# Optimization experiments

Hardware: AMD Instinct MI355X
Metric: run time of the kernel (lower is better)

The kernel has to match this reference:

```python
import jax, jax.numpy as jnp
import numpy as np

N = 100000      # nodes
E = 800000      # edges
IN1 = 128       # gcn input feature dim
IN2 = 64        # lstm input feature dim
H = 128         # hidden_channels
B = 32          # lstm batch
T = 200         # lstm seq len
OUT = 1         # out_channels
TARGET = jnp.array([0, 1000, 2000, 3000, 4000, 5000, 6000, 7000])  # numgcnE=8


def setup_inputs() -> dict:
    key = jax.random.key(0)
    ks = jax.random.split(key, 20)
    s = 0.05
    inp = {
        "data0": jax.random.normal(ks[0], (B, T, IN2), jnp.float32),
        "data1": jax.random.normal(ks[1], (N, IN1), jnp.float32),
        "edge_index": jax.random.randint(ks[2], (2, E), 0, N, dtype=jnp.int64),
        # GCNConv layers (weight stored [in, out])
        "W1": jax.random.normal(ks[3], (IN1, H), jnp.float32) * s,
        "b1": jnp.zeros((H,), jnp.float32),
        "W2": jax.random.normal(ks[4], (H, H), jnp.float32) * s,
        "b2": jnp.zeros((H,), jnp.float32),
        # LSTM1 (gate order i,f,g,o as in torch)
        "Wih1": jax.random.normal(ks[5], (4 * H, IN2), jnp.float32) * s,
        "Whh1": jax.random.normal(ks[6], (4 * H, H), jnp.float32) * s,
        "bih1": jnp.zeros((4 * H,), jnp.float32),
        "bhh1": jnp.zeros((4 * H,), jnp.float32),
        # LSTM2
        "Wih2": jax.random.normal(ks[7], (4 * H, H), jnp.float32) * s,
        "Whh2": jax.random.normal(ks[8], (4 * H, H), jnp.float32) * s,
        "bih2": jnp.zeros((4 * H,), jnp.float32),
        "bhh2": jnp.zeros((4 * H,), jnp.float32),
        # MLP head: (numgcnE+1)*H -> (numgcnE+1)*H/2 -> OUT
        "m1_w": jax.random.normal(ks[9], (9 * H, 9 * H // 2), jnp.float32) * s,
        "m1_b": jnp.zeros((9 * H // 2,), jnp.float32),
        "m2_w": jax.random.normal(ks[10], (9 * H // 2, OUT), jnp.float32) * s,
        "m2_b": jnp.zeros((OUT,), jnp.float32),
    }
    return inp


def gcn_conv(x, W, b, src, dst, n):
    # PyG GCNConv: self-loops + symmetric normalization, then scatter-add.
    xw = x @ W                                                     # [N, H]
    ones = jnp.ones(src.shape[0], xw.dtype)
    deg = jax.ops.segment_sum(ones, dst, num_segments=n) + 1.0     # +1 self-loop
    dinv = jax.lax.rsqrt(deg)                                      # [N]
    norm = dinv[src] * dinv[dst]                                   # [E]
    agg = jax.ops.segment_sum(xw[src] * norm[:, None], dst, num_segments=n)
    agg = agg + xw * (dinv * dinv)[:, None]                        # self-loop msgs
    return agg + b


def lstm_final(x_tbi, Wih, Whh, bih, bhh):
    # x_tbi: [T, Bsz, in]; returns final hidden state h_T [Bsz, H]
    Bsz = x_tbi.shape[1]
    Hh = Whh.shape[1]
    bias = bih + bhh

    def step(carry, xt):
        h, c = carry
        g = xt @ Wih.T + h @ Whh.T + bias                          # [Bsz, 4H]
        i, f, gg, o = jnp.split(g, 4, axis=-1)
        c = jax.nn.sigmoid(f) * c + jax.nn.sigmoid(i) * jnp.tanh(gg)
        h = jax.nn.sigmoid(o) * jnp.tanh(c)
        return (h, c), None

    init = (jnp.zeros((Bsz, Hh), x_tbi.dtype), jnp.zeros((Bsz, Hh), x_tbi.dtype))
    (h, c), _ = jax.lax.scan(step, init, x_tbi)
    return h


def reference(data0, data1, edge_index, W1, b1, W2, b2,
              Wih1, Whh1, bih1, bhh1, Wih2, Whh2, bih2, bhh2,
              m1_w, m1_b, m2_w, m2_b):
    src, dst = edge_index[0], edge_index[1]
    n = data1.shape[0]
    # two GCN layers with ReLU
    h = jax.nn.relu(gcn_conv(data1, W1, b1, src, dst, n))
    h = jax.nn.relu(gcn_conv(h, W2, b2, src, dst, n))
    g = h[TARGET].reshape(-1)                                      # [numgcnE*H]
    # lstm1 over [B, T, IN2] (batch_first) -> final h_n [B, H]
    h1 = lstm_final(jnp.swapaxes(data0, 0, 1), Wih1, Whh1, bih1, bhh1)
    # lstm2 consumes h_n[None] as [batch=1, seq=B, H] -> final h [1, H]
    h2 = lstm_final(h1[:, None, :], Wih2, Whh2, bih2, bhh2)[0]     # [H]
    d = jnp.concatenate([g, h2])                                   # [(numgcnE+1)*H]
    return (d @ m1_w + m1_b) @ m2_w + m2_b                         # [OUT]
```

## Files before the change

kernel.cpp:

```cpp
#include <hip/hip_runtime.h>
#include <hip/hip_bf16.h>
#include <cstring>

using bf16 = __hip_bfloat16;
typedef _Float16 h2v __attribute__((ext_vector_type(2)));
typedef _Float16 h8v __attribute__((ext_vector_type(8)));

#if __has_builtin(__builtin_amdgcn_fdot2)
__device__ __forceinline__ float FDOT2(h2v a, h2v b, float c) {
    return __builtin_amdgcn_fdot2(a, b, c, false);
}
#else
__device__ __forceinline__ float FDOT2(h2v a, h2v b, float c) {
    return c + (float)a.x * (float)b.x + (float)a.y * (float)b.y;
}
#endif

__device__ __forceinline__ float sigm_f(float x) {
    return __builtin_amdgcn_rcpf(1.f + __expf(-x));
}
__device__ __forceinline__ float tanh_f(float x) {
    return 1.f - 2.f * __builtin_amdgcn_rcpf(1.f + __expf(2.f * x));
}

constexpr int NH    = 128;
constexpr int G4    = 512;
constexpr int TSEQ  = 200;
constexpr int BBATCH= 32;
constexpr int NTGT  = 8;

constexpr int LCAP1 = 1024;
constexpr int S1CAP = LCAP1 + NTGT;
constexpr int LCAP2 = 8192;
constexpr int S2CAP = LCAP2 + S1CAP;

constexpr size_t algn(size_t x) { return (x + 255) & ~size_t(255); }
constexpr size_t OFF_GX1  = 0;
constexpr size_t OFF_GX2  = algn(OFF_GX1  + 6400ull * G4 * 4);
constexpr size_t OFF_DEG  = algn(OFF_GX2  + 32ull * G4 * 4);
constexpr size_t OFF_DINV = algn(OFF_DEG  + 100000ull * 4);
constexpr size_t OFF_SL1  = algn(OFF_DINV + 100000ull * 4);
constexpr size_t OFF_SL2  = algn(OFF_SL1  + 100000ull * 4);
constexpr size_t OFF_CNT  = algn(OFF_SL2  + 100000ull * 4);
constexpr size_t OFF_L1   = algn(OFF_CNT  + 64);
constexpr size_t OFF_S1   = algn(OFF_L1   + (size_t)LCAP1 * 8);
constexpr size_t OFF_L2   = algn(OFF_S1   + (size_t)S1CAP * 4);
constexpr size_t OFF_S2   = algn(OFF_L2   + (size_t)LCAP2 * 8);
constexpr size_t OFF_XW1  = algn(OFF_S2   + (size_t)S2CAP * 4);
constexpr size_t OFF_H1   = algn(OFF_XW1  + (size_t)S2CAP * NH * 4);
constexpr size_t OFF_XW2  = algn(OFF_H1   + (size_t)S1CAP * NH * 4);
constexpr size_t OFF_DVEC = algn(OFF_XW2  + (size_t)S1CAP * NH * 4);
constexpr size_t OFF_H1F  = algn(OFF_DVEC + 1152ull * 4);
constexpr size_t OFF_CACC = algn(OFF_H1F  + 32ull * NH * 4);
constexpr size_t WS_NEEDED = OFF_CACC + 576ull * 4;

__device__ __forceinline__ int edge_at(const int* ei, int E, int is64, int row, int e) {
    return is64 ? ei[(((size_t)row * E) + e) * 2] : ei[((size_t)row * E) + e];
}

__global__ void k_canary(unsigned int* out, unsigned int bits) {
    if (threadIdx.x == 0) out[0] = bits;
}


__global__ void k_init(const int* ei, int* deg, int* slot1, int* slot2, int* cnt,
                       float* colacc, int n) {
    int i = blockIdx.x * 256 + threadIdx.x;
    if (i < 14) cnt[i] = 0;
    if (i == 15) cnt[15] = (ei[1] == 0 && ei[3] == 0 && ei[5] == 0 && ei[7] == 0) ? 1 : 0;
    if (i < 576) colacc[i] = 0.f;
    for (; i < n; i += gridDim.x * 256) { deg[i] = 0; slot1[i] = -1; slot2[i] = -1; }
}

__global__ void k_deg_l1(const int* ei, int E, int* deg, int2* l1, int* cnt) {
    int is64 = cnt[15];
    for (int e = blockIdx.x * 256 + threadIdx.x; e < E; e += gridDim.x * 256) {
        int d = edge_at(ei, E, is64, 1, e);
        if ((unsigned)d < 100000u) atomicAdd(&deg[d], 1);
        if (d <= 7000 && d >= 0 && d % 1000 == 0) {
            int s = edge_at(ei, E, is64, 0, e);
            int idx = atomicAdd(&cnt[0], 1);
            if (idx < LCAP1) l1[idx] = make_int2(s, d);
        }
    }
}

__global__ void k_dinv(const int* deg, float* dinv, int n) {
    for (int i = blockIdx.x * 256 + threadIdx.x; i < n; i += gridDim.x * 256)
        dinv[i] = rsqrtf((float)deg[i] + 1.0f);
}

__global__ void k_s1(const int2* l1, int* cnt, int* slot1, int* s1list) {
    int m = min(cnt[0], LCAP1);
    for (int i = threadIdx.x; i < NTGT + m; i += blockDim.x) {
        int v = (i < NTGT) ? i * 1000 : l1[i - NTGT].x;
        if ((unsigned)v >= 100000u) continue;
        int old = atomicCAS(&slot1[v], -1, -2);
        if (old == -1) {
            int idx = atomicAdd(&cnt[1], 1);
            if (idx < S1CAP) { s1list[idx] = v; atomicExch(&slot1[v], idx); }
        }
    }
}

__global__ void k_s2self(const int* s1list, int* cnt, int* slot2, int* s2list) {
    int nS1 = min(cnt[1], S1CAP);
    for (int i = blockIdx.x * 256 + threadIdx.x; i < nS1; i += gridDim.x * 256) {
        int v = s1list[i];
        int old = atomicCAS(&slot2[v], -1, -2);
        if (old == -1) {
            int idx = atomicAdd(&cnt[2], 1);
            if (idx < S2CAP) { s2list[idx] = v; atomicExch(&slot2[v], idx); }
        }
    }
}

__global__ void k_l2(const int* ei, int E, const int* slot1,
                     int2* l2, int* cnt, int* slot2, int* s2list) {
    int is64 = cnt[15];
    for (int e = blockIdx.x * 256 + threadIdx.x; e < E; e += gridDim.x * 256) {
        int d = edge_at(ei, E, is64, 1, e);
        if ((unsigned)d >= 100000u) continue;
        if (slot1[d] >= 0) {
            int s = edge_at(ei, E, is64, 0, e);
            if ((unsigned)s >= 100000u) continue;
            int idx = atomicAdd(&cnt[3], 1);
            if (idx < LCAP2) l2[idx] = make_int2(s, d);
            int old = atomicCAS(&slot2[s], -1, -2);
            if (old == -1) {
                int j = atomicAdd(&cnt[2], 1);
                if (j < S2CAP) { s2list[j] = s; atomicExch(&slot2[s], j); }
            }
        }
    }
}


__global__ void k_xw1(const float* x, const float* W, const int* s2list, const int* cnt, float* xw1) {
    int i = blockIdx.x;
    if (i >= min(cnt[2], S2CAP)) return;
    int node = s2list[i];
    __shared__ float xs[NH];
    int c = threadIdx.x;
    xs[c] = x[(size_t)node * NH + c];
    __syncthreads();
    float acc = 0.f;
    #pragma unroll 8
    for (int k = 0; k < NH; k++) acc += xs[k] * W[(size_t)k * NH + c];
    xw1[(size_t)i * NH + c] = acc;
}

__global__ void k_h1init(const float* xw1, const int* s1list, const int* cnt,
                         const int* slot2, const float* dinv, float* h1) {
    int i = blockIdx.x;
    if (i >= min(cnt[1], S1CAP)) return;
    int node = s1list[i];
    int s2 = slot2[node];
    if (s2 < 0 || s2 >= S2CAP) s2 = 0;
    float v = dinv[node];
    h1[i * NH + threadIdx.x] = xw1[(size_t)s2 * NH + threadIdx.x] * v * v;
}

__global__ void k_h1scat(const float* xw1, const int2* l2, const int* cnt,
                         const int* slot1, const int* slot2, const float* dinv, float* h1) {
    int e = blockIdx.x;
    if (e >= min(cnt[3], LCAP2)) return;
    int2 sd = l2[e];
    int t1 = slot1[sd.y], s2 = slot2[sd.x];
    if (t1 < 0 || t1 >= S1CAP || s2 < 0 || s2 >= S2CAP) return;
    float w = dinv[sd.x] * dinv[sd.y];
    atomicAdd(&h1[t1 * NH + threadIdx.x],
              xw1[(size_t)s2 * NH + threadIdx.x] * w);
}

__global__ void k_xw2(const float* h1, const float* W, const float* b1, const int* cnt, float* xw2) {
    int i = blockIdx.x;
    if (i >= min(cnt[1], S1CAP)) return;
    __shared__ float xs[NH];
    int c = threadIdx.x;
    xs[c] = fmaxf(h1[i * NH + c] + b1[c], 0.f);
    __syncthreads();
    float acc = 0.f;
    #pragma unroll 8
    for (int k = 0; k < NH; k++) acc += xs[k] * W[(size_t)k * NH + c];
    xw2[(size_t)i * NH + c] = acc;
}

__global__ void k_gout(const float* xw2, const int2* l1, const int* cnt,
                       const int* slot1, const float* dinv, const float* b2, float* dvec) {
    int t = blockIdx.x;
    int tgt = t * 1000;
    int c = threadIdx.x;
    float vt = dinv[tgt];
    int st = slot1[tgt]; if (st < 0 || st >= S1CAP) st = 0;
    float acc = xw2[(size_t)st * NH + c] * vt * vt;
    int m = min(cnt[0], LCAP1);
    for (int e = 0; e < m; e++) {
        int2 sd = l1[e];
        if (sd.y == tgt) {
            int ss = slot1[sd.x];
            if (ss >= 0 && ss < S1CAP)
                acc += xw2[(size_t)ss * NH + c] * dinv[sd.x] * vt;
        }
    }
    acc += b2[c];
    dvec[t * NH + c] = fmaxf(acc, 0.f);
}


__global__ __launch_bounds__(256) void k_gx1(const float* data0, const float* Wih,
                                             const float* bih, const float* bhh, float* gx) {
    constexpr int LDP = 68;
    __shared__ float As[64 * LDP];
    __shared__ float Bs[64 * LDP];
    int tid = threadIdx.x;
    int rb = blockIdx.x >> 3;
    int gb = blockIdx.x & 7;
    int r0 = rb * 64, g0 = gb * 64;
    for (int i = tid; i < 64 * 64; i += 256) {
        int rr = i >> 6, k = i & 63;
        int r = r0 + rr, b = r & 31, t = r >> 5;
        As[rr * LDP + k] = data0[((size_t)b * TSEQ + t) * 64 + k];
        Bs[rr * LDP + k] = Wih[(size_t)(g0 + rr) * 64 + k];
    }
    __syncthreads();
    int tr = (tid & 15) * 4;
    int tg = (tid >> 4) * 4;
    float acc[4][4] = {};
    #pragma unroll
    for (int k4 = 0; k4 < 16; k4++) {
        float4 a0 = *(const float4*)&As[(tr + 0) * LDP + k4 * 4];
        float4 a1 = *(const float4*)&As[(tr + 1) * LDP + k4 * 4];
        float4 a2 = *(const float4*)&As[(tr + 2) * LDP + k4 * 4];
        float4 a3 = *(const float4*)&As[(tr + 3) * LDP + k4 * 4];
        float4 b0 = *(const float4*)&Bs[(tg + 0) * LDP + k4 * 4];
        float4 b1 = *(const float4*)&Bs[(tg + 1) * LDP + k4 * 4];
        float4 b2 = *(const float4*)&Bs[(tg + 2) * LDP + k4 * 4];
        float4 b3 = *(const float4*)&Bs[(tg + 3) * LDP + k4 * 4];
        const float4 av[4] = {a0, a1, a2, a3};
        const float4 bv[4] = {b0, b1, b2, b3};
        #pragma unroll
        for (int i = 0; i < 4; i++)
            #pragma unroll
            for (int j = 0; j < 4; j++)
                acc[i][j] += av[i].x * bv[j].x + av[i].y * bv[j].y
                           + av[i].z * bv[j].z + av[i].w * bv[j].w;
    }
    float bias[4];
    #pragma unroll
    for (int j = 0; j < 4; j++) bias[j] = bih[g0 + tg + j] + bhh[g0 + tg + j];
    #pragma unroll
    for (int i = 0; i < 4; i++) {
        size_t row = (size_t)(r0 + tr + i) * G4 + g0 + tg;
        #pragma unroll
        for (int j = 0; j < 4; j++) gx[row + j] = acc[i][j] + bias[j];
    }
}

__global__ void k_gx2(const float* h1f, const float* Wih,
                      const float* bih, const float* bhh, float* gx) {
    int t = blockIdx.x;
    __shared__ float xs[NH];
    int tid = threadIdx.x;
    int g0 = tid, g1 = tid + 256;
    if (tid < NH) xs[tid] = h1f[t * NH + tid];
    __syncthreads();
    float a0 = bih[g0] + bhh[g0];
    float a1 = bih[g1] + bhh[g1];
    #pragma unroll 4
    for (int k = 0; k < NH; k++) {
        a0 += Wih[(size_t)g0 * NH + k] * xs[k];
        a1 += Wih[(size_t)g1 * NH + k] * xs[k];
    }
    gx[(size_t)t * G4 + g0] = a0;
    gx[(size_t)t * G4 + g1] = a1;
}

template<int T, int NB>
__global__ __launch_bounds__(256, 1) void k_lstm(const float* gx, const float* Whh, float* hfinal) {
    int b = blockIdx.x;
    int t0 = threadIdx.x;
    int g0 = t0, g1 = t0 + 256;
    __shared__ __align__(16) _Float16 h2h[NH];
    __shared__ float gs[G4];
    h2v w0[NH / 2], w1[NH / 2];
    #pragma unroll
    for (int k = 0; k < NH; k += 4) {
        float4 a = *(const float4*)&Whh[(size_t)g0 * NH + k];
        w0[k / 2]     = h2v{(_Float16)a.x, (_Float16)a.y};
        w0[k / 2 + 1] = h2v{(_Float16)a.z, (_Float16)a.w};
        float4 c4 = *(const float4*)&Whh[(size_t)g1 * NH + k];
        w1[k / 2]     = h2v{(_Float16)c4.x, (_Float16)c4.y};
        w1[k / 2 + 1] = h2v{(_Float16)c4.z, (_Float16)c4.w};
    }
    if (t0 < NH) h2h[t0] = (_Float16)0.f;
    float c = 0.f, h = 0.f;
    float nx0 = gx[((size_t)0 * NB + b) * G4 + g0];
    float nx1 = gx[((size_t)0 * NB + b) * G4 + g1];
    __syncthreads();
    const h8v* hv8 = (const h8v*)h2h;
    for (int t = 0; t < T; t++) {
        float a0 = nx0, a1 = nx1;
        int tn = (t + 1 < T) ? (t + 1) : t;
        nx0 = gx[((size_t)tn * NB + b) * G4 + g0];
        nx1 = gx[((size_t)tn * NB + b) * G4 + g1];
        float p0 = 0.f, q0 = 0.f, p1 = 0.f, q1 = 0.f;
        #pragma unroll
        for (int m = 0; m < NH / 8; m++) {
            h8v h8 = hv8[m];
            h2v ha = __builtin_shufflevector(h8, h8, 0, 1);
            h2v hb = __builtin_shufflevector(h8, h8, 2, 3);
            h2v hc = __builtin_shufflevector(h8, h8, 4, 5);
            h2v hd = __builtin_shufflevector(h8, h8, 6, 7);
            p0 = FDOT2(w0[4 * m],     ha, p0);
            q0 = FDOT2(w0[4 * m + 1], hb, q0);
            p0 = FDOT2(w0[4 * m + 2], hc, p0);
            q0 = FDOT2(w0[4 * m + 3], hd, q0);
            p1 = FDOT2(w1[4 * m],     ha, p1);
            q1 = FDOT2(w1[4 * m + 1], hb, q1);
            p1 = FDOT2(w1[4 * m + 2], hc, p1);
            q1 = FDOT2(w1[4 * m + 3], hd, q1);
        }
        gs[g0] = a0 + p0 + q0;
        gs[g1] = a1 + p1 + q1;
        __syncthreads();
        if (t0 < NH) {
            int j = t0;
            float gi = gs[j], gf = gs[NH + j], gg = gs[2 * NH + j], go = gs[3 * NH + j];
            c = sigm_f(gf) * c + sigm_f(gi) * tanh_f(gg);
            h = sigm_f(go) * tanh_f(c);
            h2h[j] = (_Float16)h;
        }
        __syncthreads();
    }
    if (t0 < NH) hfinal[(size_t)b * NH + t0] = h;
}

__global__ __launch_bounds__(64) void k_head1(const float* dvec, const float* m1w, float* colacc) {
    int rg = blockIdx.x & 7;
    int cg = blockIdx.x >> 3;
    int col = cg * 64 + threadIdx.x;
    int r0 = rg * 144;
    float acc = 0.f;
    #pragma unroll 4
    for (int i = r0; i < r0 + 144; i++)
        acc += dvec[i] * m1w[(size_t)i * 576 + col];
    atomicAdd(&colacc[col], acc);
}

__global__ __launch_bounds__(256) void k_head2(const float* colacc, const float* m1b,
                                               const float* m2w, const float* m2b,
                                               unsigned int* out) {
    __shared__ float wr[4];
    int j = threadIdx.x;
    float sum = 0.f;
    for (int col = j; col < 576; col += 256)
        sum += (colacc[col] + m1b[col]) * m2w[col];
    #pragma unroll
    for (int off = 32; off > 0; off >>= 1) sum += __shfl_down(sum, off, 64);
    if ((j & 63) == 0) wr[j >> 6] = sum;
    __syncthreads();
    if (j == 0) {
        float s = wr[0] + wr[1] + wr[2] + wr[3] + m2b[0];
        bf16 hb = __float2bfloat16(s);
        unsigned short u;
        memcpy(&u, &hb, 2);
        out[0] = ((unsigned int)u << 16) | u;
    }
}


extern "C" void kernel_launch(void* const* d_in, const int* in_sizes, int n_in,
                              void* d_out, int out_size, void* d_ws, size_t ws_size,
                              hipStream_t stream) {
    const float* data0 = (const float*)d_in[0];
    const float* data1 = (const float*)d_in[1];
    const int*   ei    = (const int*)d_in[2];
    const float* W1    = (const float*)d_in[3];
    const float* b1    = (const float*)d_in[4];
    const float* W2    = (const float*)d_in[5];
    const float* b2    = (const float*)d_in[6];
    const float* Wih1  = (const float*)d_in[7];
    const float* Whh1  = (const float*)d_in[8];
    const float* bih1  = (const float*)d_in[9];
    const float* bhh1  = (const float*)d_in[10];
    const float* Wih2  = (const float*)d_in[11];
    const float* Whh2  = (const float*)d_in[12];
    const float* bih2  = (const float*)d_in[13];
    const float* bhh2  = (const float*)d_in[14];
    const float* m1w   = (const float*)d_in[15];
    const float* m1b   = (const float*)d_in[16];
    const float* m2w   = (const float*)d_in[17];
    const float* m2b   = (const float*)d_in[18];

    const int n = in_sizes[1] / NH;
    const int E = in_sizes[2] / 2;

    char* ws = (char*)d_ws;
    float* gx1   = (float*)(ws + OFF_GX1);
    float* gx2   = (float*)(ws + OFF_GX2);
    int*   deg   = (int*)  (ws + OFF_DEG);
    float* dinv  = (float*)(ws + OFF_DINV);
    int*   slot1 = (int*)  (ws + OFF_SL1);
    int*   slot2 = (int*)  (ws + OFF_SL2);
    int*   cnt   = (int*)  (ws + OFF_CNT);
    int2*  l1    = (int2*) (ws + OFF_L1);
    int*   s1l   = (int*)  (ws + OFF_S1);
    int2*  l2    = (int2*) (ws + OFF_L2);
    int*   s2l   = (int*)  (ws + OFF_S2);
    float* xw1   = (float*)(ws + OFF_XW1);
    float* h1    = (float*)(ws + OFF_H1);
    float* xw2   = (float*)(ws + OFF_XW2);
    float* dvec  = (float*)(ws + OFF_DVEC);
    float* h1f   = (float*)(ws + OFF_H1F);
    float* cacc  = (float*)(ws + OFF_CACC);

    float v = 1.0f + (ws_size < WS_NEEDED ? 1.0f : 0.0f) + (n_in != 19 ? 2.0f : 0.0f);
    unsigned int fb; memcpy(&fb, &v, 4);
    unsigned int hi = fb >> 16;
    unsigned int canary_bits = (hi << 16) | hi;
    k_canary <<<1, 64, 0, stream>>>((unsigned int*)d_out, canary_bits);

    int nb = (n + 255) / 256;
    int eb = (E + 255) / 256;

    k_init   <<<nb, 256, 0, stream>>>(ei, deg, slot1, slot2, cnt, cacc, n);
    k_deg_l1 <<<eb, 256, 0, stream>>>(ei, E, deg, l1, cnt);
    k_dinv   <<<nb, 256, 0, stream>>>(deg, dinv, n);
    k_s1     <<<1, 256, 0, stream>>>(l1, cnt, slot1, s1l);
    k_s2self <<<8, 256, 0, stream>>>(s1l, cnt, slot2, s2l);
    k_l2     <<<eb, 256, 0, stream>>>(ei, E, slot1, l2, cnt, slot2, s2l);
    k_xw1    <<<S2CAP, NH, 0, stream>>>(data1, W1, s2l, cnt, xw1);
    k_h1init <<<S1CAP, NH, 0, stream>>>(xw1, s1l, cnt, slot2, dinv, h1);
    k_h1scat <<<LCAP2, NH, 0, stream>>>(xw1, l2, cnt, slot1, slot2, dinv, h1);
    k_xw2    <<<S1CAP, NH, 0, stream>>>(h1, W2, b1, cnt, xw2);
    k_gout   <<<NTGT, NH, 0, stream>>>(xw2, l1, cnt, slot1, dinv, b2, dvec);
    k_gx1    <<<800, 256, 0, stream>>>(data0, Wih1, bih1, bhh1, gx1);
    k_lstm<TSEQ, BBATCH><<<BBATCH, 256, 0, stream>>>(gx1, Whh1, h1f);
    k_gx2    <<<BBATCH, 256, 0, stream>>>(h1f, Wih2, bih2, bhh2, gx2);
    k_lstm<BBATCH, 1>  <<<1, 256, 0, stream>>>(gx2, Whh2, dvec + 1024);
    k_head1  <<<72, 64, 0, stream>>>(dvec, m1w, cacc);
    k_head2  <<<1, 256, 0, stream>>>(cacc, m1b, m2w, m2b, (unsigned int*)d_out);
    (void)out_size;
}
```

Before: 412.2 us.

## Restructure LSTM step to one barrier via double-buffered h and shuffles; fuse small kernels

The LSTM recurrence now assigns each thread pair the four gates of one hidden unit, so gate nonlinearities run in parallel. The f and o activations are exchanged with a lane shuffle, and the hidden state is double-buffered so each timestep needs one barrier instead of two and no shared gate array. Separately, the dinv kernel is removed and rsqrt is recomputed inline from deg at each use, and k_s2self is fused into the single-block k_s1 using a shared-memory counter. These changes cut launches and per-step synchronisation in the serial 200-step chain, at the cost of some redundant rsqrt work.

```diff
diff --git a/kernel.cpp b/kernel.cpp
--- a/kernel.cpp
+++ b/kernel.cpp
@@ -58,6 +58,10 @@
     return is64 ? ei[(((size_t)row * E) + e) * 2] : ei[((size_t)row * E) + e];
 }
 
+__device__ __forceinline__ float dinv_of(const int* deg, int v) {
+    return rsqrtf((float)deg[v] + 1.0f);
+}
+
 __global__ void k_canary(unsigned int* out, unsigned int bits) {
     if (threadIdx.x == 0) out[0] = bits;
 }
@@ -85,27 +89,25 @@
     }
 }
 
-__global__ void k_dinv(const int* deg, float* dinv, int n) {
-    for (int i = blockIdx.x * 256 + threadIdx.x; i < n; i += gridDim.x * 256)
-        dinv[i] = rsqrtf((float)deg[i] + 1.0f);
-}
-
-__global__ void k_s1(const int2* l1, int* cnt, int* slot1, int* s1list) {
+__global__ void k_s1(const int2* l1, int* cnt, int* slot1, int* s1list,
+                     int* slot2, int* s2list) {
+    __shared__ int ns1;
+    if (threadIdx.x == 0) ns1 = 0;
+    __syncthreads();
     int m = min(cnt[0], LCAP1);
     for (int i = threadIdx.x; i < NTGT + m; i += blockDim.x) {
         int v = (i < NTGT) ? i * 1000 : l1[i - NTGT].x;
         if ((unsigned)v >= 100000u) continue;
         int old = atomicCAS(&slot1[v], -1, -2);
         if (old == -1) {
-            int idx = atomicAdd(&cnt[1], 1);
+            int idx = atomicAdd(&ns1, 1);
             if (idx < S1CAP) { s1list[idx] = v; atomicExch(&slot1[v], idx); }
         }
     }
-}
-
-__global__ void k_s2self(const int* s1list, int* cnt, int* slot2, int* s2list) {
-    int nS1 = min(cnt[1], S1CAP);
-    for (int i = blockIdx.x * 256 + threadIdx.x; i < nS1; i += gridDim.x * 256) {
+    __syncthreads();
+    int n1 = min(ns1, S1CAP);
+    if (threadIdx.x == 0) cnt[1] = n1;
+    for (int i = threadIdx.x; i < n1; i += blockDim.x) {
         int v = s1list[i];
         int old = atomicCAS(&slot2[v], -1, -2);
         if (old == -1) {
@@ -151,24 +153,24 @@
 }
 
 __global__ void k_h1init(const float* xw1, const int* s1list, const int* cnt,
-                         const int* slot2, const float* dinv, float* h1) {
+                         const int* slot2, const int* deg, float* h1) {
     int i = blockIdx.x;
     if (i >= min(cnt[1], S1CAP)) return;
     int node = s1list[i];
     int s2 = slot2[node];
     if (s2 < 0 || s2 >= S2CAP) s2 = 0;
-    float v = dinv[node];
+    float v = dinv_of(deg, node);
     h1[i * NH + threadIdx.x] = xw1[(size_t)s2 * NH + threadIdx.x] * v * v;
 }
 
 __global__ void k_h1scat(const float* xw1, const int2* l2, const int* cnt,
-                         const int* slot1, const int* slot2, const float* dinv, float* h1) {
+                         const int* slot1, const int* slot2, const int* deg, float* h1) {
     int e = blockIdx.x;
     if (e >= min(cnt[3], LCAP2)) return;
     int2 sd = l2[e];
     int t1 = slot1[sd.y], s2 = slot2[sd.x];
     if (t1 < 0 || t1 >= S1CAP || s2 < 0 || s2 >= S2CAP) return;
-    float w = dinv[sd.x] * dinv[sd.y];
+    float w = dinv_of(deg, sd.x) * dinv_of(deg, sd.y);
     atomicAdd(&h1[t1 * NH + threadIdx.x],
               xw1[(size_t)s2 * NH + threadIdx.x] * w);
 }
@@ -187,11 +189,11 @@
 }
 
 __global__ void k_gout(const float* xw2, const int2* l1, const int* cnt,
-                       const int* slot1, const float* dinv, const float* b2, float* dvec) {
+                       const int* slot1, const int* deg, const float* b2, float* dvec) {
     int t = blockIdx.x;
     int tgt = t * 1000;
     int c = threadIdx.x;
-    float vt = dinv[tgt];
+    float vt = dinv_of(deg, tgt);
     int st = slot1[tgt]; if (st < 0 || st >= S1CAP) st = 0;
     float acc = xw2[(size_t)st * NH + c] * vt * vt;
     int m = min(cnt[0], LCAP1);
@@ -200,7 +202,7 @@
         if (sd.y == tgt) {
             int ss = slot1[sd.x];
             if (ss >= 0 && ss < S1CAP)
-                acc += xw2[(size_t)ss * NH + c] * dinv[sd.x] * vt;
+                acc += xw2[(size_t)ss * NH + c] * dinv_of(deg, sd.x) * vt;
         }
     }
     acc += b2[c];
@@ -279,31 +281,34 @@
 template<int T, int NB>
 __global__ __launch_bounds__(256, 1) void k_lstm(const float* gx, const float* Whh, float* hfinal) {
     int b = blockIdx.x;
-    int t0 = threadIdx.x;
-    int g0 = t0, g1 = t0 + 256;
-    __shared__ __align__(16) _Float16 h2h[NH];
-    __shared__ float gs[G4];
+    int tid = threadIdx.x;
+    int w = tid >> 6, l = tid & 63;
+    int j = w * 32 + (l & 31);
+    int role = l >> 5;
+    int r0 = role ? (j + NH) : j;
+    int r1 = role ? (j + 3 * NH) : (j + 2 * NH);
+    __shared__ __align__(16) _Float16 hbuf[2][NH];
     h2v w0[NH / 2], w1[NH / 2];
     #pragma unroll
     for (int k = 0; k < NH; k += 4) {
-        float4 a = *(const float4*)&Whh[(size_t)g0 * NH + k];
+        float4 a = *(const float4*)&Whh[(size_t)r0 * NH + k];
         w0[k / 2]     = h2v{(_Float16)a.x, (_Float16)a.y};
         w0[k / 2 + 1] = h2v{(_Float16)a.z, (_Float16)a.w};
-        float4 c4 = *(const float4*)&Whh[(size_t)g1 * NH + k];
+        float4 c4 = *(const float4*)&Whh[(size_t)r1 * NH + k];
         w1[k / 2]     = h2v{(_Float16)c4.x, (_Float16)c4.y};
         w1[k / 2 + 1] = h2v{(_Float16)c4.z, (_Float16)c4.w};
     }
-    if (t0 < NH) h2h[t0] = (_Float16)0.f;
-    float c = 0.f, h = 0.f;
-    float nx0 = gx[((size_t)0 * NB + b) * G4 + g0];
-    float nx1 = gx[((size_t)0 * NB + b) * G4 + g1];
-    __syncthreads();
-    const h8v* hv8 = (const h8v*)h2h;
+    if (tid < NH) { hbuf[0][tid] = (_Float16)0.f; hbuf[1][tid] = (_Float16)0.f; }
+    float c = 0.f, hout = 0.f;
+    float nx0 = gx[((size_t)0 * NB + b) * G4 + r0];
+    float nx1 = gx[((size_t)0 * NB + b) * G4 + r1];
+    __syncthreads();
     for (int t = 0; t < T; t++) {
+        const h8v* hv8 = (const h8v*)hbuf[t & 1];
         float a0 = nx0, a1 = nx1;
         int tn = (t + 1 < T) ? (t + 1) : t;
-        nx0 = gx[((size_t)tn * NB + b) * G4 + g0];
-        nx1 = gx[((size_t)tn * NB + b) * G4 + g1];
+        nx0 = gx[((size_t)tn * NB + b) * G4 + r0];
+        nx1 = gx[((size_t)tn * NB + b) * G4 + r1];
         float p0 = 0.f, q0 = 0.f, p1 = 0.f, q1 = 0.f;
         #pragma unroll
         for (int m = 0; m < NH / 8; m++) {
@@ -321,19 +326,21 @@
             p1 = FDOT2(w1[4 * m + 2], hc, p1);
             q1 = FDOT2(w1[4 * m + 3], hd, q1);
         }
-        gs[g0] = a0 + p0 + q0;
-        gs[g1] = a1 + p1 + q1;
+        float ga = a0 + p0 + q0;
+        float gb = a1 + p1 + q1;
+        float s  = sigm_f(ga);
+        float tg = role ? sigm_f(gb) : tanh_f(gb);
+        float u  = s * tg;
+        float fv = __shfl_xor(s,  32);
+        float ov = __shfl_xor(tg, 32);
+        if (role == 0) {
+            c = fv * c + u;
+            hout = ov * tanh_f(c);
+            hbuf[(t + 1) & 1][j] = (_Float16)hout;
+        }
         __syncthreads();
-        if (t0 < NH) {
-            int j = t0;
-            float gi = gs[j], gf = gs[NH + j], gg = gs[2 * NH + j], go = gs[3 * NH + j];
-            c = sigm_f(gf) * c + sigm_f(gi) * tanh_f(gg);
-            h = sigm_f(go) * tanh_f(c);
-            h2h[j] = (_Float16)h;
-        }
-        __syncthreads();
-    }
-    if (t0 < NH) hfinal[(size_t)b * NH + t0] = h;
+    }
+    if (role == 0) hfinal[(size_t)b * NH + j] = hout;
 }
 
 __global__ __launch_bounds__(64) void k_head1(const float* dvec, const float* m1w, float* colacc) {
@@ -400,7 +407,6 @@
     float* gx1   = (float*)(ws + OFF_GX1);
     float* gx2   = (float*)(ws + OFF_GX2);
     int*   deg   = (int*)  (ws + OFF_DEG);
-    float* dinv  = (float*)(ws + OFF_DINV);
     int*   slot1 = (int*)  (ws + OFF_SL1);
     int*   slot2 = (int*)  (ws + OFF_SL2);
     int*   cnt   = (int*)  (ws + OFF_CNT);
@@ -426,15 +432,13 @@
 
     k_init   <<<nb, 256, 0, stream>>>(ei, deg, slot1, slot2, cnt, cacc, n);
     k_deg_l1 <<<eb, 256, 0, stream>>>(ei, E, deg, l1, cnt);
-    k_dinv   <<<nb, 256, 0, stream>>>(deg, dinv, n);
-    k_s1     <<<1, 256, 0, stream>>>(l1, cnt, slot1, s1l);
-    k_s2self <<<8, 256, 0, stream>>>(s1l, cnt, slot2, s2l);
+    k_s1     <<<1, 256, 0, stream>>>(l1, cnt, slot1, s1l, slot2, s2l);
     k_l2     <<<eb, 256, 0, stream>>>(ei, E, slot1, l2, cnt, slot2, s2l);
     k_xw1    <<<S2CAP, NH, 0, stream>>>(data1, W1, s2l, cnt, xw1);
-    k_h1init <<<S1CAP, NH, 0, stream>>>(xw1, s1l, cnt, slot2, dinv, h1);
-    k_h1scat <<<LCAP2, NH, 0, stream>>>(xw1, l2, cnt, slot1, slot2, dinv, h1);
+    k_h1init <<<S1CAP, NH, 0, stream>>>(xw1, s1l, cnt, slot2, deg, h1);
+    k_h1scat <<<LCAP2, NH, 0, stream>>>(xw1, l2, cnt, slot1, slot2, deg, h1);
     k_xw2    <<<S1CAP, NH, 0, stream>>>(h1, W2, b1, cnt, xw2);
-    k_gout   <<<NTGT, NH, 0, stream>>>(xw2, l1, cnt, slot1, dinv, b2, dvec);
+    k_gout   <<<NTGT, NH, 0, stream>>>(xw2, l1, cnt, slot1, deg, b2, dvec);
     k_gx1    <<<800, 256, 0, stream>>>(data0, Wih1, bih1, bhh1, gx1);
     k_lstm<TSEQ, BBATCH><<<BBATCH, 256, 0, stream>>>(gx1, Whh1, h1f);
     k_gx2    <<<BBATCH, 256, 0, stream>>>(h1f, Wih2, bih2, bhh2, gx2);
```

Result: no change. 408.9 us (-0.8%).
